# Kernel optimization log

Hardware: AMD Instinct MI355X
Metric: run time of the kernel (lower is better)

## Reference

```python
import jax, jax.numpy as jnp
import numpy as np

N = 20000   # nodes per graph
E = 320000  # edges (avg degree 16)
B = 2       # batch of graphs
D = 64      # hidden_dim
L = 25      # message-passing layers
EPS = 1e-5


def setup_inputs() -> dict:
    key = jax.random.key(0)
    ks = jax.random.split(key, 12)
    rn = lambda k, s, sc=0.05: jax.random.normal(k, s, dtype=jnp.float32) * sc
    return {
        "x_batch": jax.random.normal(ks[0], (B, N, 3), dtype=jnp.float32),
        "edge_index": jax.random.randint(ks[1], (2, E), 0, N, dtype=jnp.int32),
        "edge_attr": jax.random.normal(ks[2], (E, 2), dtype=jnp.float32),
        "enc_w": rn(ks[3], (3, D)), "enc_b": jnp.zeros((D,), jnp.float32),
        "msg_w1": rn(ks[4], (L, 2 * D + 2, D)), "msg_b1": jnp.zeros((L, D), jnp.float32),
        "msg_ln_g": jnp.ones((L, D), jnp.float32), "msg_ln_b": jnp.zeros((L, D), jnp.float32),
        "msg_w2": rn(ks[5], (L, D, D)), "msg_b2": jnp.zeros((L, D), jnp.float32),
        "up_w": rn(ks[6], (L, 2 * D, D)), "up_b": jnp.zeros((L, D), jnp.float32),
        "up_ln_g": jnp.ones((L, D), jnp.float32), "up_ln_b": jnp.zeros((L, D), jnp.float32),
        "dec_w1": rn(ks[7], (D, 32)), "dec_b1": jnp.zeros((32,), jnp.float32),
        "dec_w2": rn(ks[8], (32, 2)), "dec_b2": jnp.zeros((2,), jnp.float32),
    }


def _ln(x, g, b):
    mu = jnp.mean(x, axis=-1, keepdims=True)
    var = jnp.mean(jnp.square(x - mu), axis=-1, keepdims=True)
    return (x - mu) * jax.lax.rsqrt(var + EPS) * g + b


def reference(x_batch, edge_index, edge_attr,
              enc_w, enc_b,
              msg_w1, msg_b1, msg_ln_g, msg_ln_b, msg_w2, msg_b2,
              up_w, up_b, up_ln_g, up_ln_b,
              dec_w1, dec_b1, dec_w2, dec_b2):
    row, col = edge_index[0], edge_index[1]
    layer_params = (msg_w1, msg_b1, msg_ln_g, msg_ln_b, msg_w2, msg_b2,
                    up_w, up_b, up_ln_g, up_ln_b)

    def step(h, p):  # h: [N, D]
        w1, b1, g1, be1, w2, b2, uw, ub, ug, ube = p
        cat = jnp.concatenate([h[row], h[col], edge_attr], axis=1)  # [E, 2D+2]
        m = jax.nn.relu(_ln(cat @ w1 + b1, g1, be1)) @ w2 + b2      # [E, D]
        aggr = jax.ops.segment_sum(m, row, num_segments=N)          # [N, D]
        u = jax.nn.relu(_ln(jnp.concatenate([h, aggr], axis=1) @ uw + ub, ug, ube))
        return h + u, None

    def graph(x):  # x: [N, 3]
        h0 = x @ enc_w + enc_b
        h, _ = jax.lax.scan(step, h0, layer_params)
        return jax.nn.relu(h @ dec_w1 + dec_b1) @ dec_w2 + dec_b2  # [N, 2]

    return jax.vmap(graph)(x_batch)  # [B, N, 2]
```

## Files before the change

### kernel.cpp

```cpp
#include <hip/hip_runtime.h>

constexpr int N = 20000;
constexpr int E = 320000;
constexpr int Bc = 2;
constexpr int D = 64;
constexpr int L = 25;
constexpr float EPS = 1e-5f;

typedef __attribute__((ext_vector_type(8))) short short8;
typedef __attribute__((ext_vector_type(4))) float f32x4;

__device__ __forceinline__ unsigned short f2bf(float f) {
  unsigned u = __float_as_uint(f);
  u += 0x7fff + ((u >> 16) & 1);
  return (unsigned short)(u >> 16);
}

__global__ void hist_kernel(const int* __restrict__ row, int* __restrict__ deg) {
  int e = blockIdx.x * blockDim.x + threadIdx.x;
  if (e < E) atomicAdd(&deg[row[e]], 1);
}

__global__ __launch_bounds__(1024) void scan_kernel(const int* __restrict__ deg,
                                                    int* __restrict__ row_start,
                                                    int* __restrict__ cursor) {
  __shared__ int s[1024];
  const int t = threadIdx.x;
  constexpr int CH = (N + 1023) / 1024;
  int base = t * CH;
  int sum = 0;
  for (int k = 0; k < CH; ++k) {
    int idx = base + k;
    if (idx < N) sum += deg[idx];
  }
  s[t] = sum;
  __syncthreads();
  for (int off = 1; off < 1024; off <<= 1) {
    int v = (t >= off) ? s[t - off] : 0;
    __syncthreads();
    s[t] += v;
    __syncthreads();
  }
  int excl = s[t] - sum;
  for (int k = 0; k < CH; ++k) {
    int idx = base + k;
    if (idx < N) {
      row_start[idx] = excl;
      cursor[idx] = excl;
      excl += deg[idx];
    }
  }
  if (t == 1023) row_start[N] = s[1023];
}

__global__ void scatter_kernel(const int* __restrict__ row, int* __restrict__ cursor,
                               int* __restrict__ edge_order) {
  int e = blockIdx.x * blockDim.x + threadIdx.x;
  if (e < E) {
    int p = atomicAdd(&cursor[row[e]], 1);
    edge_order[p] = e;
  }
}

__global__ void sortmap_kernel(const int* __restrict__ edge_order,
                               const int* __restrict__ col,
                               const float* __restrict__ eattr,
                               int* __restrict__ col_s, float2* __restrict__ ea_s) {
  int p = blockIdx.x * blockDim.x + threadIdx.x;
  if (p < E) {
    int eid = edge_order[p];
    col_s[p] = col[eid];
    ea_s[p] = *(const float2*)&eattr[2 * (size_t)eid];
  }
}

__global__ __launch_bounds__(512) void packuw_kernel(
    const float* __restrict__ up_w, unsigned short* __restrict__ uwpack) {
  const int f = blockIdx.x;
  const int l = blockIdx.y;
  const int t = threadIdx.x;
  const int ln = t >> 3, i = t & 7;
  int nt = f >> 2, ks = f & 3;
  int k = ks * 32 + (ln >> 4) * 8 + i, n = nt * 16 + (ln & 15);
  uwpack[((size_t)l * 16 + f) * 512 + ln * 8 + i] =
      f2bf(up_w[(size_t)l * 128 * 64 + (size_t)k * 64 + n]);
}

__global__ __launch_bounds__(512) void encoder_kernel(
    const float* __restrict__ x, const float* __restrict__ enc_w,
    const float* __restrict__ enc_b, float* __restrict__ h,
    unsigned short* __restrict__ hbf) {
  int idx = blockIdx.x * blockDim.x + threadIdx.x;
  if (idx >= Bc * N * D) return;
  int j = idx & (D - 1);
  int bn = idx >> 6;
  const float* xp = x + (size_t)bn * 3;
  float v = enc_b[j] + xp[0] * enc_w[j] + xp[1] * enc_w[D + j] + xp[2] * enc_w[2 * D + j];
  h[idx] = v;
  hbf[idx] = f2bf(v);
}

constexpr int GPN = 4;
constexpr int GPG = N / GPN;
constexpr int NGRP = GPG * Bc;
constexpr int EWB = 8;
constexpr int ETPB = EWB * 64;

__global__ __launch_bounds__(ETPB, 4) void layer_kernel(
    const unsigned short* __restrict__ hbf_old, unsigned short* __restrict__ hbf_new,
    float* __restrict__ h,
    const int* __restrict__ col_s, const float2* __restrict__ ea_s,
    const int* __restrict__ row_start,
    const float* __restrict__ w1, const float* __restrict__ b1,
    const float* __restrict__ g1, const float* __restrict__ be1,
    const float* __restrict__ w2, const float* __restrict__ b2,
    const unsigned short* __restrict__ uwpack_l, const float* __restrict__ ub,
    const float* __restrict__ ug, const float* __restrict__ ube) {
  __shared__ __align__(16) char smem[24576 + EWB * 3072];
  unsigned short* w1f = (unsigned short*)smem;
  unsigned short* w2f = (unsigned short*)(smem + 16384);

  const int tid = threadIdx.x, lane = tid & 63, w = tid >> 6;
  const int cl = lane & 15, hg = lane >> 4;
  char* pw = smem + 24576 + w * 3072;
  float* aggs = (float*)(pw + 2048);

  for (int idx = tid; idx < 16 * 512; idx += ETPB) {
    int f = idx >> 9, rem = idx & 511, ln = rem >> 3, i = rem & 7;
    int nt = f >> 2, ks = f & 3;
    int k = ks * 32 + (ln >> 4) * 8 + i, n = nt * 16 + (ln & 15);
    w1f[idx] = f2bf(w1[k * 64 + n]);
  }
  for (int idx = tid; idx < 8 * 512; idx += ETPB) {
    int f = idx >> 9, rem = idx & 511, ln = rem >> 3, i = rem & 7;
    int nt = f >> 1, ks = f & 1;
    int k = ks * 32 + (ln >> 4) * 8 + i, n = nt * 16 + (ln & 15);
    w2f[idx] = f2bf(w2[k * 64 + n]);
  }
  __syncthreads();

  float b1c[4], g1c[4], be1c[4], b2c[4], wA[4], wB[4], ubc[4], ugc[4], ubec[4];
#pragma unroll
  for (int nt = 0; nt < 4; ++nt) {
    int c = nt * 16 + cl;
    b1c[nt] = b1[c]; g1c[nt] = g1[c]; be1c[nt] = be1[c]; b2c[nt] = b2[c];
    wA[nt] = w1[128 * 64 + c]; wB[nt] = w1[129 * 64 + c];
    ubc[nt] = ub[c]; ugc[nt] = ug[c]; ubec[nt] = ube[c];
  }
  const short8* w1v = (const short8*)w1f;
  const short8* w2v = (const short8*)w2f;
  const short8* uwv = (const short8*)uwpack_l;

  const int gw = __builtin_amdgcn_readfirstlane(blockIdx.x * EWB + w);
  if (gw >= NGRP) return;
  const int g = (gw >= GPG) ? 1 : 0;
  const int nb = (gw - g * GPG) * GPN;
  const unsigned short* hb = hbf_old + (size_t)g * N * 64;

  int rs[GPN + 1];
#pragma unroll
  for (int k = 0; k <= GPN; ++k) rs[k] = row_start[nb + k];

#pragma unroll
  for (int k = 0; k < GPN; ++k) aggs[k * 64 + lane] = 0.f;

  for (int k = 0; k < GPN; ++k) {
    const int es = rs[k], ee = rs[k + 1];
    const int deg = ee - es;
    if (deg == 0) continue;
    float macc[4] = {0.f, 0.f, 0.f, 0.f};

    const unsigned short* pn = hb + (((size_t)(nb + k)) << 6) + hg * 8;
    const short8 av0 = *(const short8*)pn;
    const short8 av1 = *(const short8*)(pn + 32);

    int pos = es + cl; if (pos >= ee) pos = ee - 1;
    float2 eaC = ea_s[pos];
    const unsigned short* pc0 = hb + (((size_t)col_s[pos]) << 6) + hg * 8;
    short8 a2C = *(const short8*)pc0;
    short8 a3C = *(const short8*)(pc0 + 32);

    for (int ts = es; ts < ee; ts += 16) {
      const bool hasN = (ts + 16) < ee;
      float2 eaN; short8 a2N, a3N;
      if (hasN) {
        int p2 = ts + 16 + cl; if (p2 >= ee) p2 = ee - 1;
        eaN = ea_s[p2];
        const unsigned short* pc = hb + (((size_t)col_s[p2]) << 6) + hg * 8;
        a2N = *(const short8*)pc;
        a3N = *(const short8*)(pc + 32);
      }

      f32x4 acc[4];
#pragma unroll
      for (int nt = 0; nt < 4; ++nt) acc[nt] = (f32x4){0.f, 0.f, 0.f, 0.f};
      __builtin_amdgcn_s_setprio(1);
#pragma unroll
      for (int nt = 0; nt < 4; ++nt)
        acc[nt] = __builtin_amdgcn_mfma_f32_16x16x32_bf16(av0, w1v[(nt * 4 + 0) * 64 + lane], acc[nt], 0, 0, 0);
#pragma unroll
      for (int nt = 0; nt < 4; ++nt)
        acc[nt] = __builtin_amdgcn_mfma_f32_16x16x32_bf16(av1, w1v[(nt * 4 + 1) * 64 + lane], acc[nt], 0, 0, 0);
#pragma unroll
      for (int nt = 0; nt < 4; ++nt)
        acc[nt] = __builtin_amdgcn_mfma_f32_16x16x32_bf16(a2C, w1v[(nt * 4 + 2) * 64 + lane], acc[nt], 0, 0, 0);
#pragma unroll
      for (int nt = 0; nt < 4; ++nt)
        acc[nt] = __builtin_amdgcn_mfma_f32_16x16x32_bf16(a3C, w1v[(nt * 4 + 3) * 64 + lane], acc[nt], 0, 0, 0);
      __builtin_amdgcn_s_setprio(0);

#pragma unroll
      for (int r = 0; r < 4; ++r) {
        const int edge = hg * 4 + r;
        float e0 = __shfl(eaC.x, edge, 64);
        float e1 = __shfl(eaC.y, edge, 64);
        float v[4];
#pragma unroll
        for (int nt = 0; nt < 4; ++nt)
          v[nt] = acc[nt][r] + b1c[nt] + e0 * wA[nt] + e1 * wB[nt];
        float s = v[0] + v[1] + v[2] + v[3];
        float q = v[0] * v[0] + v[1] * v[1] + v[2] * v[2] + v[3] * v[3];
#pragma unroll
        for (int o = 1; o < 16; o <<= 1) {
          s += __shfl_xor(s, o, 64);
          q += __shfl_xor(q, o, 64);
        }
        float mu = s * (1.f / 64.f);
        float var = fmaf(-mu, mu, q * (1.f / 64.f));
        float rsq = rsqrtf(var + EPS);
#pragma unroll
        for (int nt = 0; nt < 4; ++nt) {
          float p = fmaxf((v[nt] - mu) * rsq * g1c[nt] + be1c[nt], 0.f);
          unsigned byteoff = (unsigned)(edge * 128 + (nt * 16 + cl) * 2) ^ (unsigned)(hg << 5);
          *(unsigned short*)(pw + byteoff) = f2bf(p);
        }
      }

      f32x4 m[4];
#pragma unroll
      for (int nt = 0; nt < 4; ++nt) m[nt] = (f32x4){0.f, 0.f, 0.f, 0.f};
      __builtin_amdgcn_s_setprio(1);
#pragma unroll
      for (int ks = 0; ks < 2; ++ks) {
        unsigned byteoff = (unsigned)(cl * 128 + (ks * 32 + hg * 8) * 2) ^ (unsigned)((cl >> 2) << 5);
        short8 a2 = *(const short8*)(pw + byteoff);
#pragma unroll
        for (int nt = 0; nt < 4; ++nt)
          m[nt] = __builtin_amdgcn_mfma_f32_16x16x32_bf16(
              a2, w2v[(nt * 2 + ks) * 64 + lane], m[nt], 0, 0, 0);
      }
      __builtin_amdgcn_s_setprio(0);

      const int vleft = ee - ts - hg * 4;
#pragma unroll
      for (int r = 0; r < 4; ++r) {
        if (r < vleft) {
#pragma unroll
          for (int nt = 0; nt < 4; ++nt) macc[nt] += m[nt][r];
        }
      }

      if (hasN) { eaC = eaN; a2C = a2N; a3C = a3N; }
    }

    float fin[4];
#pragma unroll
    for (int nt = 0; nt < 4; ++nt) {
      float s = macc[nt];
      s += __shfl_xor(s, 16, 64);
      s += __shfl_xor(s, 32, 64);
      fin[nt] = s + (float)deg * b2c[nt];
    }
    float sv = (hg == 0) ? fin[0] : (hg == 1) ? fin[1] : (hg == 2) ? fin[2] : fin[3];
    aggs[k * 64 + ((hg * 16 + cl) ^ (k << 3))] = sv;
  }

  {
    const int nc = (cl < GPN) ? cl : (GPN - 1);
    const unsigned short* ph = hb + (((size_t)(nb + nc)) << 6) + hg * 8;
    short8 av[4];
    av[0] = *(const short8*)ph;
    av[1] = *(const short8*)(ph + 32);
    const int i0 = nc * 64 + ((hg * 8) ^ (nc << 3));
    const int i1 = nc * 64 + (((32 + hg * 8)) ^ (nc << 3));
    float4 q0 = *(const float4*)&aggs[i0];
    float4 q1 = *(const float4*)&aggs[i0 + 4];
    float4 q2 = *(const float4*)&aggs[i1];
    float4 q3 = *(const float4*)&aggs[i1 + 4];
    {
      union { short8 s; unsigned short u[8]; } t2, t3;
      t2.u[0] = f2bf(q0.x); t2.u[1] = f2bf(q0.y); t2.u[2] = f2bf(q0.z); t2.u[3] = f2bf(q0.w);
      t2.u[4] = f2bf(q1.x); t2.u[5] = f2bf(q1.y); t2.u[6] = f2bf(q1.z); t2.u[7] = f2bf(q1.w);
      t3.u[0] = f2bf(q2.x); t3.u[1] = f2bf(q2.y); t3.u[2] = f2bf(q2.z); t3.u[3] = f2bf(q2.w);
      t3.u[4] = f2bf(q3.x); t3.u[5] = f2bf(q3.y); t3.u[6] = f2bf(q3.z); t3.u[7] = f2bf(q3.w);
      av[2] = t2.s; av[3] = t3.s;
    }

    f32x4 acc[4];
#pragma unroll
    for (int nt = 0; nt < 4; ++nt) acc[nt] = (f32x4){0.f, 0.f, 0.f, 0.f};
    __builtin_amdgcn_s_setprio(1);
#pragma unroll
    for (int ks = 0; ks < 4; ++ks) {
#pragma unroll
      for (int nt = 0; nt < 4; ++nt)
        acc[nt] = __builtin_amdgcn_mfma_f32_16x16x32_bf16(
            av[ks], uwv[(nt * 4 + ks) * 64 + lane], acc[nt], 0, 0, 0);
    }
    __builtin_amdgcn_s_setprio(0);

#pragma unroll
    for (int r = 0; r < 4; ++r) {
      float v[4];
#pragma unroll
      for (int nt = 0; nt < 4; ++nt) v[nt] = acc[nt][r] + ubc[nt];
      float s = v[0] + v[1] + v[2] + v[3];
      float q = v[0] * v[0] + v[1] * v[1] + v[2] * v[2] + v[3] * v[3];
#pragma unroll
      for (int o = 1; o < 16; o <<= 1) {
        s += __shfl_xor(s, o, 64);
        q += __shfl_xor(q, o, 64);
      }
      float mu = s * (1.f / 64.f);
      float var = fmaf(-mu, mu, q * (1.f / 64.f));
      float rsq = rsqrtf(var + EPS);
      if (hg == 0) {
        const size_t nrow = ((size_t)(g * N + nb + r)) << 6;
#pragma unroll
        for (int nt = 0; nt < 4; ++nt) {
          int c = nt * 16 + cl;
          float u = fmaxf((v[nt] - mu) * rsq * ugc[nt] + ubec[nt], 0.f);
          float nv = h[nrow + c] + u;
          h[nrow + c] = nv;
          hbf_new[nrow + c] = f2bf(nv);
        }
      }
    }
  }
}

__global__ __launch_bounds__(512) void decoder_kernel(
    const float* __restrict__ h,
    const float* __restrict__ dw1, const float* __restrict__ db1,
    const float* __restrict__ dw2, const float* __restrict__ db2,
    float* __restrict__ out) {
  __shared__ __align__(16) float w1s[64 * 32];
  __shared__ float w2s[64];
  __shared__ float b1s[32];
  __shared__ float hs[8][64];
  const int tid = threadIdx.x;
  const int lane = tid & 63;
  const int w = tid >> 6;

  for (int idx = tid; idx < 64 * 32; idx += 512) w1s[idx] = dw1[idx];
  if (tid < 64) w2s[tid] = dw2[tid];
  if (tid < 32) b1s[tid] = db1[tid];
  const float ob0 = db2[0], ob1 = db2[1];
  __syncthreads();

  const int total = Bc * N;
  const int per_iter = gridDim.x * 8;
  const int niter = (total + per_iter - 1) / per_iter;
  const int wave_global = blockIdx.x * 8 + w;

  for (int it = 0; it < niter; ++it) {
    const int i = it * per_iter + wave_global;
    if (i < total) {
      hs[w][lane] = h[((size_t)i << 6) + lane];
      float s1 = 0.f;
      if (lane < 32) {
        s1 = b1s[lane];
        for (int k = 0; k < 64; ++k) s1 = fmaf(hs[w][k], w1s[k * 32 + lane], s1);
        s1 = fmaxf(s1, 0.f);
      }
      float c0 = (lane < 32) ? s1 * w2s[lane * 2]     : 0.f;
      float c1 = (lane < 32) ? s1 * w2s[lane * 2 + 1] : 0.f;
#pragma unroll
      for (int off = 16; off > 0; off >>= 1) {
        c0 += __shfl_xor(c0, off, 64);
        c1 += __shfl_xor(c1, off, 64);
      }
      if (lane == 0) {
        out[(size_t)i * 2]     = c0 + ob0;
        out[(size_t)i * 2 + 1] = c1 + ob1;
      }
    }
  }
}

extern "C" void kernel_launch(void* const* d_in, const int* in_sizes, int n_in,
                              void* d_out, int out_size, void* d_ws, size_t ws_size,
                              hipStream_t stream) {
  const float* x        = (const float*)d_in[0];
  const int*   ei       = (const int*)d_in[1];
  const float* eattr    = (const float*)d_in[2];
  const float* enc_w    = (const float*)d_in[3];
  const float* enc_b    = (const float*)d_in[4];
  const float* msg_w1   = (const float*)d_in[5];
  const float* msg_b1   = (const float*)d_in[6];
  const float* msg_ln_g = (const float*)d_in[7];
  const float* msg_ln_b = (const float*)d_in[8];
  const float* msg_w2   = (const float*)d_in[9];
  const float* msg_b2   = (const float*)d_in[10];
  const float* up_w     = (const float*)d_in[11];
  const float* up_b     = (const float*)d_in[12];
  const float* up_ln_g  = (const float*)d_in[13];
  const float* up_ln_b  = (const float*)d_in[14];
  const float* dw1      = (const float*)d_in[15];
  const float* db1      = (const float*)d_in[16];
  const float* dw2      = (const float*)d_in[17];
  const float* db2      = (const float*)d_in[18];
  float* out = (float*)d_out;

  float* h              = (float*)d_ws;
  unsigned short* hbf0  = (unsigned short*)(h + (size_t)Bc * N * D);
  unsigned short* hbf1  = hbf0 + (size_t)Bc * N * D;
  unsigned short* uwpack = hbf1 + (size_t)Bc * N * D;
  float2* ea_sv         = (float2*)(uwpack + (size_t)L * 16 * 512);
  int* col_sv           = (int*)(ea_sv + E);
  int* edge_order       = col_sv + E;
  int* deg              = edge_order + E;
  int* row_start        = deg + N;
  int* cursor           = row_start + N + 1;

  const int* row = ei;
  const int* col = ei + E;

  hipMemsetAsync(deg, 0, N * sizeof(int), stream);
  hist_kernel<<<(E + 255) / 256, 256, 0, stream>>>(row, deg);
  scan_kernel<<<1, 1024, 0, stream>>>(deg, row_start, cursor);
  scatter_kernel<<<(E + 255) / 256, 256, 0, stream>>>(row, cursor, edge_order);
  sortmap_kernel<<<(E + 255) / 256, 256, 0, stream>>>(edge_order, col, eattr, col_sv, ea_sv);
  packuw_kernel<<<dim3(16, L), 512, 0, stream>>>(up_w, uwpack);
  encoder_kernel<<<(Bc * N * D + 511) / 512, 512, 0, stream>>>(x, enc_w, enc_b, h, hbf0);

  unsigned short* hbufs[2] = {hbf0, hbf1};
  for (int l = 0; l < L; ++l) {
    layer_kernel<<<(NGRP + EWB - 1) / EWB, ETPB, 0, stream>>>(
        hbufs[l & 1], hbufs[(l + 1) & 1], h,
        col_sv, ea_sv, row_start,
        msg_w1 + (size_t)l * 130 * 64, msg_b1 + l * 64,
        msg_ln_g + l * 64, msg_ln_b + l * 64,
        msg_w2 + (size_t)l * 64 * 64, msg_b2 + l * 64,
        uwpack + (size_t)l * 16 * 512, up_b + l * 64,
        up_ln_g + l * 64, up_ln_b + l * 64);
  }

  decoder_kernel<<<512, 512, 0, stream>>>(h, dw1, db1, dw2, db2, out);
}
```

Before: 2.446 ms.

## Prepack all layer weights once and use persistent grid-stride layer blocks

Extends the one-time weight packing kernel to convert msg_w1 and msg_w2 into the bf16 MFMA fragment layout for all layers. Each layer block then copies its weights into shared memory with plain uint4 loads instead of doing per-element conversion. The layer kernel also switches from one block per 32 node-groups to a fixed grid of 768 blocks that loop over groups. This amortises the per-block weight staging over many groups, at the risk of load imbalance across the persistent blocks.

```diff
diff --git a/kernel.cpp b/kernel.cpp
--- a/kernel.cpp
+++ b/kernel.cpp
@@ -74,16 +74,28 @@
   }
 }
 
-__global__ __launch_bounds__(512) void packuw_kernel(
-    const float* __restrict__ up_w, unsigned short* __restrict__ uwpack) {
+__global__ __launch_bounds__(512) void packw_kernel(
+    const float* __restrict__ msg_w1, const float* __restrict__ msg_w2,
+    const float* __restrict__ up_w, unsigned short* __restrict__ wpack) {
   const int f = blockIdx.x;
   const int l = blockIdx.y;
   const int t = threadIdx.x;
   const int ln = t >> 3, i = t & 7;
-  int nt = f >> 2, ks = f & 3;
-  int k = ks * 32 + (ln >> 4) * 8 + i, n = nt * 16 + (ln & 15);
-  uwpack[((size_t)l * 16 + f) * 512 + ln * 8 + i] =
-      f2bf(up_w[(size_t)l * 128 * 64 + (size_t)k * 64 + n]);
+  float v;
+  if (f < 16) {
+    int nt = f >> 2, ks = f & 3;
+    int k = ks * 32 + (ln >> 4) * 8 + i, n = nt * 16 + (ln & 15);
+    v = msg_w1[(size_t)l * 130 * 64 + (size_t)k * 64 + n];
+  } else if (f < 24) {
+    int f2 = f - 16, nt = f2 >> 1, ks = f2 & 1;
+    int k = ks * 32 + (ln >> 4) * 8 + i, n = nt * 16 + (ln & 15);
+    v = msg_w2[(size_t)l * 64 * 64 + (size_t)k * 64 + n];
+  } else {
+    int f3 = f - 24, nt = f3 >> 2, ks = f3 & 3;
+    int k = ks * 32 + (ln >> 4) * 8 + i, n = nt * 16 + (ln & 15);
+    v = up_w[(size_t)l * 128 * 64 + (size_t)k * 64 + n];
+  }
+  wpack[((size_t)l * 40 + f) * 512 + ln * 8 + i] = f2bf(v);
 }
 
 __global__ __launch_bounds__(512) void encoder_kernel(
@@ -105,16 +117,17 @@
 constexpr int NGRP = GPG * Bc;
 constexpr int EWB = 8;
 constexpr int ETPB = EWB * 64;
+constexpr int GRID = 768;
 
 __global__ __launch_bounds__(ETPB, 4) void layer_kernel(
     const unsigned short* __restrict__ hbf_old, unsigned short* __restrict__ hbf_new,
     float* __restrict__ h,
     const int* __restrict__ col_s, const float2* __restrict__ ea_s,
     const int* __restrict__ row_start,
+    const unsigned short* __restrict__ wpack_l,
     const float* __restrict__ w1, const float* __restrict__ b1,
     const float* __restrict__ g1, const float* __restrict__ be1,
-    const float* __restrict__ w2, const float* __restrict__ b2,
-    const unsigned short* __restrict__ uwpack_l, const float* __restrict__ ub,
+    const float* __restrict__ b2, const float* __restrict__ ub,
     const float* __restrict__ ug, const float* __restrict__ ube) {
   __shared__ __align__(16) char smem[24576 + EWB * 3072];
   unsigned short* w1f = (unsigned short*)smem;
@@ -125,17 +138,10 @@
   char* pw = smem + 24576 + w * 3072;
   float* aggs = (float*)(pw + 2048);
 
-  for (int idx = tid; idx < 16 * 512; idx += ETPB) {
-    int f = idx >> 9, rem = idx & 511, ln = rem >> 3, i = rem & 7;
-    int nt = f >> 2, ks = f & 3;
-    int k = ks * 32 + (ln >> 4) * 8 + i, n = nt * 16 + (ln & 15);
-    w1f[idx] = f2bf(w1[k * 64 + n]);
-  }
-  for (int idx = tid; idx < 8 * 512; idx += ETPB) {
-    int f = idx >> 9, rem = idx & 511, ln = rem >> 3, i = rem & 7;
-    int nt = f >> 1, ks = f & 1;
-    int k = ks * 32 + (ln >> 4) * 8 + i, n = nt * 16 + (ln & 15);
-    w2f[idx] = f2bf(w2[k * 64 + n]);
+  {
+    const uint4* src = (const uint4*)wpack_l;
+    uint4* dst = (uint4*)smem;
+    for (int idx = tid; idx < 1536; idx += ETPB) dst[idx] = src[idx];
   }
   __syncthreads();
 
@@ -149,46 +155,151 @@
   }
   const short8* w1v = (const short8*)w1f;
   const short8* w2v = (const short8*)w2f;
-  const short8* uwv = (const short8*)uwpack_l;
-
-  const int gw = __builtin_amdgcn_readfirstlane(blockIdx.x * EWB + w);
-  if (gw >= NGRP) return;
-  const int g = (gw >= GPG) ? 1 : 0;
-  const int nb = (gw - g * GPG) * GPN;
-  const unsigned short* hb = hbf_old + (size_t)g * N * 64;
-
-  int rs[GPN + 1];
-#pragma unroll
-  for (int k = 0; k <= GPN; ++k) rs[k] = row_start[nb + k];
-
-#pragma unroll
-  for (int k = 0; k < GPN; ++k) aggs[k * 64 + lane] = 0.f;
-
-  for (int k = 0; k < GPN; ++k) {
-    const int es = rs[k], ee = rs[k + 1];
-    const int deg = ee - es;
-    if (deg == 0) continue;
-    float macc[4] = {0.f, 0.f, 0.f, 0.f};
-
-    const unsigned short* pn = hb + (((size_t)(nb + k)) << 6) + hg * 8;
-    const short8 av0 = *(const short8*)pn;
-    const short8 av1 = *(const short8*)(pn + 32);
-
-    int pos = es + cl; if (pos >= ee) pos = ee - 1;
-    float2 eaC = ea_s[pos];
-    const unsigned short* pc0 = hb + (((size_t)col_s[pos]) << 6) + hg * 8;
-    short8 a2C = *(const short8*)pc0;
-    short8 a3C = *(const short8*)(pc0 + 32);
-
-    for (int ts = es; ts < ee; ts += 16) {
-      const bool hasN = (ts + 16) < ee;
-      float2 eaN; short8 a2N, a3N;
-      if (hasN) {
-        int p2 = ts + 16 + cl; if (p2 >= ee) p2 = ee - 1;
-        eaN = ea_s[p2];
-        const unsigned short* pc = hb + (((size_t)col_s[p2]) << 6) + hg * 8;
-        a2N = *(const short8*)pc;
-        a3N = *(const short8*)(pc + 32);
+  const short8* uwv = (const short8*)(wpack_l + 24 * 512);
+
+  for (int gwb = blockIdx.x * EWB + w; gwb < NGRP; gwb += GRID * EWB) {
+    const int gw = __builtin_amdgcn_readfirstlane(gwb);
+    const int g = (gw >= GPG) ? 1 : 0;
+    const int nb = (gw - g * GPG) * GPN;
+    const unsigned short* hb = hbf_old + (size_t)g * N * 64;
+
+    int rs[GPN + 1];
+#pragma unroll
+    for (int k = 0; k <= GPN; ++k) rs[k] = row_start[nb + k];
+
+#pragma unroll
+    for (int k = 0; k < GPN; ++k) aggs[k * 64 + lane] = 0.f;
+
+    for (int k = 0; k < GPN; ++k) {
+      const int es = rs[k], ee = rs[k + 1];
+      const int deg = ee - es;
+      if (deg == 0) continue;
+      float macc[4] = {0.f, 0.f, 0.f, 0.f};
+
+      const unsigned short* pn = hb + (((size_t)(nb + k)) << 6) + hg * 8;
+      const short8 av0 = *(const short8*)pn;
+      const short8 av1 = *(const short8*)(pn + 32);
+
+      int pos = es + cl; if (pos >= ee) pos = ee - 1;
+      float2 eaC = ea_s[pos];
+      const unsigned short* pc0 = hb + (((size_t)col_s[pos]) << 6) + hg * 8;
+      short8 a2C = *(const short8*)pc0;
+      short8 a3C = *(const short8*)(pc0 + 32);
+
+      for (int ts = es; ts < ee; ts += 16) {
+        const bool hasN = (ts + 16) < ee;
+        float2 eaN; short8 a2N, a3N;
+        if (hasN) {
+          int p2 = ts + 16 + cl; if (p2 >= ee) p2 = ee - 1;
+          eaN = ea_s[p2];
+          const unsigned short* pc = hb + (((size_t)col_s[p2]) << 6) + hg * 8;
+          a2N = *(const short8*)pc;
+          a3N = *(const short8*)(pc + 32);
+        }
+
+        f32x4 acc[4];
+#pragma unroll
+        for (int nt = 0; nt < 4; ++nt) acc[nt] = (f32x4){0.f, 0.f, 0.f, 0.f};
+        __builtin_amdgcn_s_setprio(1);
+#pragma unroll
+        for (int nt = 0; nt < 4; ++nt)
+          acc[nt] = __builtin_amdgcn_mfma_f32_16x16x32_bf16(av0, w1v[(nt * 4 + 0) * 64 + lane], acc[nt], 0, 0, 0);
+#pragma unroll
+        for (int nt = 0; nt < 4; ++nt)
+          acc[nt] = __builtin_amdgcn_mfma_f32_16x16x32_bf16(av1, w1v[(nt * 4 + 1) * 64 + lane], acc[nt], 0, 0, 0);
+#pragma unroll
+        for (int nt = 0; nt < 4; ++nt)
+          acc[nt] = __builtin_amdgcn_mfma_f32_16x16x32_bf16(a2C, w1v[(nt * 4 + 2) * 64 + lane], acc[nt], 0, 0, 0);
+#pragma unroll
+        for (int nt = 0; nt < 4; ++nt)
+          acc[nt] = __builtin_amdgcn_mfma_f32_16x16x32_bf16(a3C, w1v[(nt * 4 + 3) * 64 + lane], acc[nt], 0, 0, 0);
+        __builtin_amdgcn_s_setprio(0);
+
+#pragma unroll
+        for (int r = 0; r < 4; ++r) {
+          const int edge = hg * 4 + r;
+          float e0 = __shfl(eaC.x, edge, 64);
+          float e1 = __shfl(eaC.y, edge, 64);
+          float v[4];
+#pragma unroll
+          for (int nt = 0; nt < 4; ++nt)
+            v[nt] = acc[nt][r] + b1c[nt] + e0 * wA[nt] + e1 * wB[nt];
+          float s = v[0] + v[1] + v[2] + v[3];
+          float q = v[0] * v[0] + v[1] * v[1] + v[2] * v[2] + v[3] * v[3];
+#pragma unroll
+          for (int o = 1; o < 16; o <<= 1) {
+            s += __shfl_xor(s, o, 64);
+            q += __shfl_xor(q, o, 64);
+          }
+          float mu = s * (1.f / 64.f);
+          float var = fmaf(-mu, mu, q * (1.f / 64.f));
+          float rsq = rsqrtf(var + EPS);
+#pragma unroll
+          for (int nt = 0; nt < 4; ++nt) {
+            float p = fmaxf((v[nt] - mu) * rsq * g1c[nt] + be1c[nt], 0.f);
+            unsigned byteoff = (unsigned)(edge * 128 + (nt * 16 + cl) * 2) ^ (unsigned)(hg << 5);
+            *(unsigned short*)(pw + byteoff) = f2bf(p);
+          }
+        }
+
+        f32x4 m[4];
+#pragma unroll
+        for (int nt = 0; nt < 4; ++nt) m[nt] = (f32x4){0.f, 0.f, 0.f, 0.f};
+        __builtin_amdgcn_s_setprio(1);
+#pragma unroll
+        for (int ks = 0; ks < 2; ++ks) {
+          unsigned byteoff = (unsigned)(cl * 128 + (ks * 32 + hg * 8) * 2) ^ (unsigned)((cl >> 2) << 5);
+          short8 a2 = *(const short8*)(pw + byteoff);
+#pragma unroll
+          for (int nt = 0; nt < 4; ++nt)
+            m[nt] = __builtin_amdgcn_mfma_f32_16x16x32_bf16(
+                a2, w2v[(nt * 2 + ks) * 64 + lane], m[nt], 0, 0, 0);
+        }
+        __builtin_amdgcn_s_setprio(0);
+
+        const int vleft = ee - ts - hg * 4;
+#pragma unroll
+        for (int r = 0; r < 4; ++r) {
+          if (r < vleft) {
+#pragma unroll
+            for (int nt = 0; nt < 4; ++nt) macc[nt] += m[nt][r];
+          }
+        }
+
+        if (hasN) { eaC = eaN; a2C = a2N; a3C = a3N; }
+      }
+
+      float fin[4];
+#pragma unroll
+      for (int nt = 0; nt < 4; ++nt) {
+        float s = macc[nt];
+        s += __shfl_xor(s, 16, 64);
+        s += __shfl_xor(s, 32, 64);
+        fin[nt] = s + (float)deg * b2c[nt];
+      }
+      float sv = (hg == 0) ? fin[0] : (hg == 1) ? fin[1] : (hg == 2) ? fin[2] : fin[3];
+      aggs[k * 64 + ((hg * 16 + cl) ^ (k << 3))] = sv;
+    }
+
+    {
+      const int nc = (cl < GPN) ? cl : (GPN - 1);
+      const unsigned short* ph = hb + (((size_t)(nb + nc)) << 6) + hg * 8;
+      short8 av[4];
+      av[0] = *(const short8*)ph;
+      av[1] = *(const short8*)(ph + 32);
+      const int i0 = nc * 64 + ((hg * 8) ^ (nc << 3));
+      const int i1 = nc * 64 + (((32 + hg * 8)) ^ (nc << 3));
+      float4 q0 = *(const float4*)&aggs[i0];
+      float4 q1 = *(const float4*)&aggs[i0 + 4];
+      float4 q2 = *(const float4*)&aggs[i1];
+      float4 q3 = *(const float4*)&aggs[i1 + 4];
+      {
+        union { short8 s; unsigned short u[8]; } t2, t3;
+        t2.u[0] = f2bf(q0.x); t2.u[1] = f2bf(q0.y); t2.u[2] = f2bf(q0.z); t2.u[3] = f2bf(q0.w);
+        t2.u[4] = f2bf(q1.x); t2.u[5] = f2bf(q1.y); t2.u[6] = f2bf(q1.z); t2.u[7] = f2bf(q1.w);
+        t3.u[0] = f2bf(q2.x); t3.u[1] = f2bf(q2.y); t3.u[2] = f2bf(q2.z); t3.u[3] = f2bf(q2.w);
+        t3.u[4] = f2bf(q3.x); t3.u[5] = f2bf(q3.y); t3.u[6] = f2bf(q3.z); t3.u[7] = f2bf(q3.w);
+        av[2] = t2.s; av[3] = t3.s;
       }
 
       f32x4 acc[4];
@@ -196,28 +307,19 @@
       for (int nt = 0; nt < 4; ++nt) acc[nt] = (f32x4){0.f, 0.f, 0.f, 0.f};
       __builtin_amdgcn_s_setprio(1);
 #pragma unroll
-      for (int nt = 0; nt < 4; ++nt)
-        acc[nt] = __builtin_amdgcn_mfma_f32_16x16x32_bf16(av0, w1v[(nt * 4 + 0) * 64 + lane], acc[nt], 0, 0, 0);
-#pragma unroll
-      for (int nt = 0; nt < 4; ++nt)
-        acc[nt] = __builtin_amdgcn_mfma_f32_16x16x32_bf16(av1, w1v[(nt * 4 + 1) * 64 + lane], acc[nt], 0, 0, 0);
-#pragma unroll
-      for (int nt = 0; nt < 4; ++nt)
-        acc[nt] = __builtin_amdgcn_mfma_f32_16x16x32_bf16(a2C, w1v[(nt * 4 + 2) * 64 + lane], acc[nt], 0, 0, 0);
-#pragma unroll
-      for (int nt = 0; nt < 4; ++nt)
-        acc[nt] = __builtin_amdgcn_mfma_f32_16x16x32_bf16(a3C, w1v[(nt * 4 + 3) * 64 + lane], acc[nt], 0, 0, 0);
+      for (int ks = 0; ks < 4; ++ks) {
+#pragma unroll
+        for (int nt = 0; nt < 4; ++nt)
+          acc[nt] = __builtin_amdgcn_mfma_f32_16x16x32_bf16(
+              av[ks], uwv[(nt * 4 + ks) * 64 + lane], acc[nt], 0, 0, 0);
+      }
       __builtin_amdgcn_s_setprio(0);
 
 #pragma unroll
       for (int r = 0; r < 4; ++r) {
-        const int edge = hg * 4 + r;
-        float e0 = __shfl(eaC.x, edge, 64);
-        float e1 = __shfl(eaC.y, edge, 64);
         float v[4];
 #pragma unroll
-        for (int nt = 0; nt < 4; ++nt)
-          v[nt] = acc[nt][r] + b1c[nt] + e0 * wA[nt] + e1 * wB[nt];
+        for (int nt = 0; nt < 4; ++nt) v[nt] = acc[nt][r] + ubc[nt];
         float s = v[0] + v[1] + v[2] + v[3];
         float q = v[0] * v[0] + v[1] * v[1] + v[2] * v[2] + v[3] * v[3];
 #pragma unroll
@@ -228,111 +330,16 @@
         float mu = s * (1.f / 64.f);
         float var = fmaf(-mu, mu, q * (1.f / 64.f));
         float rsq = rsqrtf(var + EPS);
-#pragma unroll
-        for (int nt = 0; nt < 4; ++nt) {
-          float p = fmaxf((v[nt] - mu) * rsq * g1c[nt] + be1c[nt], 0.f);
-          unsigned byteoff = (unsigned)(edge * 128 + (nt * 16 + cl) * 2) ^ (unsigned)(hg << 5);
-          *(unsigned short*)(pw + byteoff) = f2bf(p);
-        }
-      }
-
-      f32x4 m[4];
-#pragma unroll
-      for (int nt = 0; nt < 4; ++nt) m[nt] = (f32x4){0.f, 0.f, 0.f, 0.f};
-      __builtin_amdgcn_s_setprio(1);
-#pragma unroll
-      for (int ks = 0; ks < 2; ++ks) {
-        unsigned byteoff = (unsigned)(cl * 128 + (ks * 32 + hg * 8) * 2) ^ (unsigned)((cl >> 2) << 5);
-        short8 a2 = *(const short8*)(pw + byteoff);
-#pragma unroll
-        for (int nt = 0; nt < 4; ++nt)
-          m[nt] = __builtin_amdgcn_mfma_f32_16x16x32_bf16(
-              a2, w2v[(nt * 2 + ks) * 64 + lane], m[nt], 0, 0, 0);
-      }
-      __builtin_amdgcn_s_setprio(0);
-
-      const int vleft = ee - ts - hg * 4;
-#pragma unroll
-      for (int r = 0; r < 4; ++r) {
-        if (r < vleft) {
-#pragma unroll
-          for (int nt = 0; nt < 4; ++nt) macc[nt] += m[nt][r];
-        }
-      }
-
-      if (hasN) { eaC = eaN; a2C = a2N; a3C = a3N; }
-    }
-
-    float fin[4];
-#pragma unroll
-    for (int nt = 0; nt < 4; ++nt) {
-      float s = macc[nt];
-      s += __shfl_xor(s, 16, 64);
-      s += __shfl_xor(s, 32, 64);
-      fin[nt] = s + (float)deg * b2c[nt];
-    }
-    float sv = (hg == 0) ? fin[0] : (hg == 1) ? fin[1] : (hg == 2) ? fin[2] : fin[3];
-    aggs[k * 64 + ((hg * 16 + cl) ^ (k << 3))] = sv;
-  }
-
-  {
-    const int nc = (cl < GPN) ? cl : (GPN - 1);
-    const unsigned short* ph = hb + (((size_t)(nb + nc)) << 6) + hg * 8;
-    short8 av[4];
-    av[0] = *(const short8*)ph;
-    av[1] = *(const short8*)(ph + 32);
-    const int i0 = nc * 64 + ((hg * 8) ^ (nc << 3));
-    const int i1 = nc * 64 + (((32 + hg * 8)) ^ (nc << 3));
-    float4 q0 = *(const float4*)&aggs[i0];
-    float4 q1 = *(const float4*)&aggs[i0 + 4];
-    float4 q2 = *(const float4*)&aggs[i1];
-    float4 q3 = *(const float4*)&aggs[i1 + 4];
-    {
-      union { short8 s; unsigned short u[8]; } t2, t3;
-      t2.u[0] = f2bf(q0.x); t2.u[1] = f2bf(q0.y); t2.u[2] = f2bf(q0.z); t2.u[3] = f2bf(q0.w);
-      t2.u[4] = f2bf(q1.x); t2.u[5] = f2bf(q1.y); t2.u[6] = f2bf(q1.z); t2.u[7] = f2bf(q1.w);
-      t3.u[0] = f2bf(q2.x); t3.u[1] = f2bf(q2.y); t3.u[2] = f2bf(q2.z); t3.u[3] = f2bf(q2.w);
-      t3.u[4] = f2bf(q3.x); t3.u[5] = f2bf(q3.y); t3.u[6] = f2bf(q3.z); t3.u[7] = f2bf(q3.w);
-      av[2] = t2.s; av[3] = t3.s;
-    }
-
-    f32x4 acc[4];
-#pragma unroll
-    for (int nt = 0; nt < 4; ++nt) acc[nt] = (f32x4){0.f, 0.f, 0.f, 0.f};
-    __builtin_amdgcn_s_setprio(1);
-#pragma unroll
-    for (int ks = 0; ks < 4; ++ks) {
-#pragma unroll
-      for (int nt = 0; nt < 4; ++nt)
-        acc[nt] = __builtin_amdgcn_mfma_f32_16x16x32_bf16(
-            av[ks], uwv[(nt * 4 + ks) * 64 + lane], acc[nt], 0, 0, 0);
-    }
-    __builtin_amdgcn_s_setprio(0);
-
-#pragma unroll
-    for (int r = 0; r < 4; ++r) {
-      float v[4];
-#pragma unroll
-      for (int nt = 0; nt < 4; ++nt) v[nt] = acc[nt][r] + ubc[nt];
-      float s = v[0] + v[1] + v[2] + v[3];
-      float q = v[0] * v[0] + v[1] * v[1] + v[2] * v[2] + v[3] * v[3];
-#pragma unroll
-      for (int o = 1; o < 16; o <<= 1) {
-        s += __shfl_xor(s, o, 64);
-        q += __shfl_xor(q, o, 64);
-      }
-      float mu = s * (1.f / 64.f);
-      float var = fmaf(-mu, mu, q * (1.f / 64.f));
-      float rsq = rsqrtf(var + EPS);
-      if (hg == 0) {
-        const size_t nrow = ((size_t)(g * N + nb + r)) << 6;
-#pragma unroll
-        for (int nt = 0; nt < 4; ++nt) {
-          int c = nt * 16 + cl;
-          float u = fmaxf((v[nt] - mu) * rsq * ugc[nt] + ubec[nt], 0.f);
-          float nv = h[nrow + c] + u;
-          h[nrow + c] = nv;
-          hbf_new[nrow + c] = f2bf(nv);
+        if (hg == 0) {
+          const size_t nrow = ((size_t)(g * N + nb + r)) << 6;
+#pragma unroll
+          for (int nt = 0; nt < 4; ++nt) {
+            int c = nt * 16 + cl;
+            float u = fmaxf((v[nt] - mu) * rsq * ugc[nt] + ubec[nt], 0.f);
+            float nv = h[nrow + c] + u;
+            h[nrow + c] = nv;
+            hbf_new[nrow + c] = f2bf(nv);
+          }
         }
       }
     }
@@ -415,8 +422,8 @@
   float* h              = (float*)d_ws;
   unsigned short* hbf0  = (unsigned short*)(h + (size_t)Bc * N * D);
   unsigned short* hbf1  = hbf0 + (size_t)Bc * N * D;
-  unsigned short* uwpack = hbf1 + (size_t)Bc * N * D;
-  float2* ea_sv         = (float2*)(uwpack + (size_t)L * 16 * 512);
+  unsigned short* wpack = hbf1 + (size_t)Bc * N * D;
+  float2* ea_sv         = (float2*)(wpack + (size_t)L * 40 * 512);
   int* col_sv           = (int*)(ea_sv + E);
   int* edge_order       = col_sv + E;
   int* deg              = edge_order + E;
@@ -431,18 +438,18 @@
   scan_kernel<<<1, 1024, 0, stream>>>(deg, row_start, cursor);
   scatter_kernel<<<(E + 255) / 256, 256, 0, stream>>>(row, cursor, edge_order);
   sortmap_kernel<<<(E + 255) / 256, 256, 0, stream>>>(edge_order, col, eattr, col_sv, ea_sv);
-  packuw_kernel<<<dim3(16, L), 512, 0, stream>>>(up_w, uwpack);
+  packw_kernel<<<dim3(40, L), 512, 0, stream>>>(msg_w1, msg_w2, up_w, wpack);
   encoder_kernel<<<(Bc * N * D + 511) / 512, 512, 0, stream>>>(x, enc_w, enc_b, h, hbf0);
 
   unsigned short* hbufs[2] = {hbf0, hbf1};
   for (int l = 0; l < L; ++l) {
-    layer_kernel<<<(NGRP + EWB - 1) / EWB, ETPB, 0, stream>>>(
+    layer_kernel<<<GRID, ETPB, 0, stream>>>(
         hbufs[l & 1], hbufs[(l + 1) & 1], h,
         col_sv, ea_sv, row_start,
+        wpack + (size_t)l * 40 * 512,
         msg_w1 + (size_t)l * 130 * 64, msg_b1 + l * 64,
         msg_ln_g + l * 64, msg_ln_b + l * 64,
-        msg_w2 + (size_t)l * 64 * 64, msg_b2 + l * 64,
-        uwpack + (size_t)l * 16 * 512, up_b + l * 64,
+        msg_b2 + l * 64, up_b + l * 64,
         up_ln_g + l * 64, up_ln_b + l * 64);
   }
 
```

New measurement: 3.113 ms. 1.27x slower.

## Apply message second linear after segment sum instead of per edge

Applied to the files above, without the earlier changes.

Uses linearity, sum_e(relu(...) @ W2 + b2) = (sum_e relu(...)) @ W2 + deg*b2, to accumulate the post-LayerNorm ReLU activations per node and run the W2 MFMA once per node group rather than per 16-edge tile. This removes the per-edge LDS staging of bf16 activations, the second MFMA pass in the edge loop, and per-warp shared memory. Rounding changes because the summed activations are converted to bf16 before the matmul, which may reduce accuracy for high-degree nodes.

```diff
diff --git a/kernel.cpp b/kernel.cpp
--- a/kernel.cpp
+++ b/kernel.cpp
@@ -116,14 +116,13 @@
     const float* __restrict__ w2, const float* __restrict__ b2,
     const unsigned short* __restrict__ uwpack_l, const float* __restrict__ ub,
     const float* __restrict__ ug, const float* __restrict__ ube) {
-  __shared__ __align__(16) char smem[24576 + EWB * 3072];
+  __shared__ __align__(16) char smem[24576 + EWB * 1024];
   unsigned short* w1f = (unsigned short*)smem;
   unsigned short* w2f = (unsigned short*)(smem + 16384);
 
   const int tid = threadIdx.x, lane = tid & 63, w = tid >> 6;
   const int cl = lane & 15, hg = lane >> 4;
-  char* pw = smem + 24576 + w * 3072;
-  float* aggs = (float*)(pw + 2048);
+  float* aggs = (float*)(smem + 24576 + w * 1024);
 
   for (int idx = tid; idx < 16 * 512; idx += ETPB) {
     int f = idx >> 9, rem = idx & 511, ln = rem >> 3, i = rem & 7;
@@ -166,8 +165,7 @@
 
   for (int k = 0; k < GPN; ++k) {
     const int es = rs[k], ee = rs[k + 1];
-    const int deg = ee - es;
-    if (deg == 0) continue;
+    if (ee == es) continue;
     float macc[4] = {0.f, 0.f, 0.f, 0.f};
 
     const unsigned short* pn = hb + (((size_t)(nb + k)) << 6) + hg * 8;
@@ -209,6 +207,7 @@
         acc[nt] = __builtin_amdgcn_mfma_f32_16x16x32_bf16(a3C, w1v[(nt * 4 + 3) * 64 + lane], acc[nt], 0, 0, 0);
       __builtin_amdgcn_s_setprio(0);
 
+      const int vleft = ee - ts - hg * 4;
 #pragma unroll
       for (int r = 0; r < 4; ++r) {
         const int edge = hg * 4 + r;
@@ -228,35 +227,10 @@
         float mu = s * (1.f / 64.f);
         float var = fmaf(-mu, mu, q * (1.f / 64.f));
         float rsq = rsqrtf(var + EPS);
-#pragma unroll
-        for (int nt = 0; nt < 4; ++nt) {
-          float p = fmaxf((v[nt] - mu) * rsq * g1c[nt] + be1c[nt], 0.f);
-          unsigned byteoff = (unsigned)(edge * 128 + (nt * 16 + cl) * 2) ^ (unsigned)(hg << 5);
-          *(unsigned short*)(pw + byteoff) = f2bf(p);
-        }
-      }
-
-      f32x4 m[4];
-#pragma unroll
-      for (int nt = 0; nt < 4; ++nt) m[nt] = (f32x4){0.f, 0.f, 0.f, 0.f};
-      __builtin_amdgcn_s_setprio(1);
-#pragma unroll
-      for (int ks = 0; ks < 2; ++ks) {
-        unsigned byteoff = (unsigned)(cl * 128 + (ks * 32 + hg * 8) * 2) ^ (unsigned)((cl >> 2) << 5);
-        short8 a2 = *(const short8*)(pw + byteoff);
-#pragma unroll
-        for (int nt = 0; nt < 4; ++nt)
-          m[nt] = __builtin_amdgcn_mfma_f32_16x16x32_bf16(
-              a2, w2v[(nt * 2 + ks) * 64 + lane], m[nt], 0, 0, 0);
-      }
-      __builtin_amdgcn_s_setprio(0);
-
-      const int vleft = ee - ts - hg * 4;
-#pragma unroll
-      for (int r = 0; r < 4; ++r) {
         if (r < vleft) {
 #pragma unroll
-          for (int nt = 0; nt < 4; ++nt) macc[nt] += m[nt][r];
+          for (int nt = 0; nt < 4; ++nt)
+            macc[nt] += fmaxf((v[nt] - mu) * rsq * g1c[nt] + be1c[nt], 0.f);
         }
       }
 
@@ -269,10 +243,52 @@
       float s = macc[nt];
       s += __shfl_xor(s, 16, 64);
       s += __shfl_xor(s, 32, 64);
-      fin[nt] = s + (float)deg * b2c[nt];
+      fin[nt] = s;
     }
     float sv = (hg == 0) ? fin[0] : (hg == 1) ? fin[1] : (hg == 2) ? fin[2] : fin[3];
     aggs[k * 64 + ((hg * 16 + cl) ^ (k << 3))] = sv;
+  }
+
+  {
+    const int nc = (cl < GPN) ? cl : (GPN - 1);
+    const int i0 = nc * 64 + ((hg * 8) ^ (nc << 3));
+    const int i1 = nc * 64 + ((32 + hg * 8) ^ (nc << 3));
+    float4 q0 = *(const float4*)&aggs[i0];
+    float4 q1 = *(const float4*)&aggs[i0 + 4];
+    float4 q2 = *(const float4*)&aggs[i1];
+    float4 q3 = *(const float4*)&aggs[i1 + 4];
+    short8 p0, p1;
+    {
+      union { short8 s; unsigned short u[8]; } t0, t1;
+      t0.u[0] = f2bf(q0.x); t0.u[1] = f2bf(q0.y); t0.u[2] = f2bf(q0.z); t0.u[3] = f2bf(q0.w);
+      t0.u[4] = f2bf(q1.x); t0.u[5] = f2bf(q1.y); t0.u[6] = f2bf(q1.z); t0.u[7] = f2bf(q1.w);
+      t1.u[0] = f2bf(q2.x); t1.u[1] = f2bf(q2.y); t1.u[2] = f2bf(q2.z); t1.u[3] = f2bf(q2.w);
+      t1.u[4] = f2bf(q3.x); t1.u[5] = f2bf(q3.y); t1.u[6] = f2bf(q3.z); t1.u[7] = f2bf(q3.w);
+      p0 = t0.s; p1 = t1.s;
+    }
+
+    f32x4 agg[4];
+    __builtin_amdgcn_s_setprio(1);
+#pragma unroll
+    for (int nt = 0; nt < 4; ++nt) {
+      f32x4 t = __builtin_amdgcn_mfma_f32_16x16x32_bf16(
+          p0, w2v[(nt * 2 + 0) * 64 + lane], (f32x4){0.f, 0.f, 0.f, 0.f}, 0, 0, 0);
+      agg[nt] = __builtin_amdgcn_mfma_f32_16x16x32_bf16(
+          p1, w2v[(nt * 2 + 1) * 64 + lane], t, 0, 0, 0);
+    }
+    __builtin_amdgcn_s_setprio(0);
+
+    if (hg == 0) {
+#pragma unroll
+      for (int r = 0; r < 4; ++r) {
+        const float degf = (float)(rs[r + 1] - rs[r]);
+#pragma unroll
+        for (int nt = 0; nt < 4; ++nt) {
+          int c = nt * 16 + cl;
+          aggs[r * 64 + (c ^ (r << 3))] = agg[nt][r] + degf * b2c[nt];
+        }
+      }
+    }
   }
 
   {
@@ -282,7 +298,7 @@
     av[0] = *(const short8*)ph;
     av[1] = *(const short8*)(ph + 32);
     const int i0 = nc * 64 + ((hg * 8) ^ (nc << 3));
-    const int i1 = nc * 64 + (((32 + hg * 8)) ^ (nc << 3));
+    const int i1 = nc * 64 + ((32 + hg * 8) ^ (nc << 3));
     float4 q0 = *(const float4*)&aggs[i0];
     float4 q1 = *(const float4*)&aggs[i0 + 4];
     float4 q2 = *(const float4*)&aggs[i1];
```

Result: slower. 3.904 ms (+59.6%).
